# Performance work log

Hardware: AMD Instinct MI355X
Metric: run time of the kernel (lower is better)

Reference implementation:

```python
import jax, jax.numpy as jnp
import numpy as np

NUM_Q = 1000
NUM_PID = 5000
DIM_S = 128
SIZE_M = 50
B, T = 64, 200


def setup_inputs() -> dict:
    key = jax.random.key(0)
    ks = jax.random.split(key, 16)
    s = 1.0 / np.sqrt(DIM_S)
    inp = {
        "q": jax.random.randint(ks[0], (B, T), 0, NUM_Q),
        "r": jax.random.randint(ks[1], (B, T), 0, 2),
        "pid": jax.random.randint(ks[2], (B, T), 0, NUM_PID),
        "pid_emb": jax.random.normal(ks[3], (NUM_PID, DIM_S), jnp.float32),
        "k_emb": jax.random.normal(ks[4], (NUM_Q, DIM_S), jnp.float32),
        "v_emb": jax.random.normal(ks[5], (NUM_Q * 2, DIM_S), jnp.float32),
        "Mk": jax.random.normal(ks[6], (SIZE_M, DIM_S), jnp.float32) * np.sqrt(2.0 / DIM_S),
        "Mv0": jax.random.normal(ks[7], (SIZE_M, DIM_S), jnp.float32) * np.sqrt(2.0 / DIM_S),
        "f_W": jax.random.normal(ks[8], (DIM_S, 2 * DIM_S), jnp.float32) * s,
        "f_b": jnp.zeros((DIM_S,), jnp.float32),
        "p_W": jax.random.normal(ks[9], (1, DIM_S), jnp.float32) * s,
        "p_b": jnp.zeros((1,), jnp.float32),
        "e_W": jax.random.normal(ks[10], (DIM_S, DIM_S), jnp.float32) * s,
        "e_b": jnp.zeros((DIM_S,), jnp.float32),
        "a_W": jax.random.normal(ks[11], (DIM_S, DIM_S), jnp.float32) * s,
        "a_b": jnp.zeros((DIM_S,), jnp.float32),
    }
    return inp


def reference(q, r, pid, pid_emb, k_emb, v_emb, Mk, Mv0, f_W, f_b, p_W, p_b, e_W, e_b, a_W, a_b):
    x = q + NUM_Q * r                         # [B,T] combined q/answer index
    p_e = pid_emb[pid]                        # [B,T,D]
    k = k_emb[q] + p_e                        # [B,T,D]
    v = v_emb[x] + p_e                        # [B,T,D]
    w = jax.nn.softmax(jnp.einsum("btd,md->btm", k, Mk), axis=-1)  # [B,T,M]
    e = jax.nn.sigmoid(jnp.einsum("btd,od->bto", v, e_W) + e_b)    # [B,T,D]
    a = jnp.tanh(jnp.einsum("btd,od->bto", v, a_W) + a_b)          # [B,T,D]

    def step(Mvt, wea):
        wt, et, at = wea                      # [B,M], [B,D], [B,D]
        we = wt[:, :, None]
        Mvt = Mvt * (1.0 - we * et[:, None, :]) + we * at[:, None, :]
        return Mvt, Mvt

    Mv0_b = jnp.broadcast_to(Mv0, (q.shape[0], SIZE_M, DIM_S))
    _, Mv_seq = jax.lax.scan(
        step, Mv0_b,
        (jnp.swapaxes(w, 0, 1), jnp.swapaxes(e, 0, 1), jnp.swapaxes(a, 0, 1)))
    Mv = jnp.concatenate([Mv0_b[:, None], jnp.swapaxes(Mv_seq, 0, 1)], axis=1)  # [B,T+1,M,D]

    read = jnp.einsum("btm,btmd->btd", w, Mv[:, :-1])   # read before each write
    f = jnp.tanh(jnp.einsum("btd,od->bto", jnp.concatenate([read, k], axis=-1), f_W) + f_b)
    p = jax.nn.sigmoid(jnp.einsum("btd,od->bto", f, p_W) + p_b)[..., 0]  # [B,T]
    return (p, Mv)
```

## Files before the change

### kernel.cpp

```cpp
#include <hip/hip_runtime.h>
#include <math.h>

#define BB 64
#define TT 200
#define NUMQ 1000
#define DIMS 128
#define SIZEM 50
#define NROWS (BB*TT)
#define NCH 8
#define CL  25

__global__ __launch_bounds__(256) void k_kernel(
    const int* __restrict__ qv, const int* __restrict__ pidv,
    const float* __restrict__ k_emb, const float* __restrict__ pid_emb,
    float* __restrict__ kout)
{
    int i = blockIdx.x * 256 + threadIdx.x;
    int row = i >> 5;
    int d4  = i & 31;
    int qq = qv[row];
    int pp = pidv[row];
    float4 kvv = ((const float4*)(k_emb  + (size_t)qq * DIMS))[d4];
    float4 pvv = ((const float4*)(pid_emb + (size_t)pp * DIMS))[d4];
    float4 o;
    o.x = kvv.x + pvv.x; o.y = kvv.y + pvv.y;
    o.z = kvv.z + pvv.z; o.w = kvv.w + pvv.w;
    ((float4*)kout)[i] = o;
}

__global__ __launch_bounds__(256) void w_kernel(
    const float* __restrict__ k, const float* __restrict__ Mk,
    float* __restrict__ wout)
{
    __shared__ float MkT[DIMS * SIZEM];
    int tid = threadIdx.x;
    for (int idx = tid; idx < SIZEM * DIMS; idx += 256) {
        int m = idx >> 7;
        int d = idx & 127;
        MkT[d * SIZEM + m] = Mk[idx];
    }
    __syncthreads();

    int wave = tid >> 6;
    int lane = tid & 63;
    int m = (lane < SIZEM) ? lane : (SIZEM - 1);
    int gw = blockIdx.x * 4 + wave;

    for (int row = gw; row < NROWS; row += 256 * 4) {
        const float* kr = k + (size_t)row * DIMS;
        float acc = 0.f;
        #pragma unroll 4
        for (int d = 0; d < DIMS; d++) {
            acc = fmaf(kr[d], MkT[d * SIZEM + m], acc);
        }
        float val = (lane < SIZEM) ? acc : -INFINITY;
        #pragma unroll
        for (int off = 32; off >= 1; off >>= 1)
            val = fmaxf(val, __shfl_xor(val, off));
        float ex = (lane < SIZEM) ? __expf(acc - val) : 0.f;
        float s = ex;
        #pragma unroll
        for (int off = 32; off >= 1; off >>= 1)
            s += __shfl_xor(s, off);
        if (lane < SIZEM)
            wout[(size_t)row * SIZEM + lane] = ex / s;
    }
}

__global__ __launch_bounds__(256) void ea_kernel(
    const int* __restrict__ qv, const int* __restrict__ rv, const int* __restrict__ pidv,
    const float* __restrict__ v_emb, const float* __restrict__ pid_emb,
    const float* __restrict__ e_W, const float* __restrict__ e_b,
    const float* __restrict__ a_W, const float* __restrict__ a_b,
    float* __restrict__ e_out, float* __restrict__ a_out)
{
    __shared__ float vb[32][DIMS];
    int tid = threadIdx.x;
    int o   = tid & 127;
    int sel = tid >> 7;
    int r0  = blockIdx.x * 32;

    for (int idx = tid; idx < 32 * DIMS; idx += 256) {
        int r = idx >> 7, d = idx & 127;
        int row = r0 + r;
        int x = qv[row] + NUMQ * rv[row];
        vb[r][d] = v_emb[(size_t)x * DIMS + d] + pid_emb[(size_t)pidv[row] * DIMS + d];
    }
    __syncthreads();

    float acc[32];
    #pragma unroll
    for (int r = 0; r < 32; r++) acc[r] = 0.f;

    const float* W = sel ? a_W : e_W;
    const float* wrow = W + (size_t)o * DIMS;
    for (int d = 0; d < DIMS; d += 4) {
        float4 wv = *(const float4*)(wrow + d);
        #pragma unroll
        for (int r = 0; r < 32; r++) {
            float4 v4 = *(const float4*)(&vb[r][d]);
            acc[r] = fmaf(v4.x, wv.x, acc[r]);
            acc[r] = fmaf(v4.y, wv.y, acc[r]);
            acc[r] = fmaf(v4.z, wv.z, acc[r]);
            acc[r] = fmaf(v4.w, wv.w, acc[r]);
        }
    }
    float bo = sel ? a_b[o] : e_b[o];
    float* outp = sel ? a_out : e_out;
    #pragma unroll
    for (int r = 0; r < 32; r++) {
        float x = acc[r] + bo;
        float y = sel ? tanhf(x) : 1.f / (1.f + __expf(-x));
        outp[(size_t)(r0 + r) * DIMS + o] = y;
    }
}

__global__ __launch_bounds__(128) void compose_kernel(
    const float* __restrict__ w, const float* __restrict__ e, const float* __restrict__ a,
    float* __restrict__ Abuf, float* __restrict__ Bbuf)
{
    int b = blockIdx.x >> 3;
    int c = blockIdx.x & 7;
    int d = threadIdx.x;

    float A[SIZEM], Bv[SIZEM];
    #pragma unroll
    for (int m = 0; m < SIZEM; m++) { A[m] = 1.f; Bv[m] = 0.f; }

    const float* wr = w + ((size_t)b * TT + c * CL) * SIZEM;
    const float* er = e + ((size_t)b * TT + c * CL) * DIMS + d;
    const float* ar = a + ((size_t)b * TT + c * CL) * DIMS + d;

    for (int t = 0; t < CL; t++) {
        float ed = er[(size_t)t * DIMS];
        float ad = ar[(size_t)t * DIMS];
        const float* wt = wr + (size_t)t * SIZEM;
        #pragma unroll
        for (int m = 0; m < SIZEM; m++) {
            float wv = wt[m];
            float t1 = wv * ed;
            A[m]  = fmaf(-A[m], t1, A[m]);
            Bv[m] = fmaf(-Bv[m], t1, fmaf(wv, ad, Bv[m]));
        }
    }
    float* Ao = Abuf + ((size_t)b * NCH + c) * SIZEM * DIMS + d;
    float* Bo = Bbuf + ((size_t)b * NCH + c) * SIZEM * DIMS + d;
    #pragma unroll
    for (int m = 0; m < SIZEM; m++) {
        Ao[(size_t)m * DIMS] = A[m];
        Bo[(size_t)m * DIMS] = Bv[m];
    }
}

__global__ __launch_bounds__(256) void boundary_kernel(
    const float* __restrict__ Abuf, const float* __restrict__ Bbuf,
    const float* __restrict__ Mv0, float* __restrict__ sstart)
{
    int b = blockIdx.x / 25;
    int g = blockIdx.x % 25;
    int flat = g * 256 + threadIdx.x;
    float s = Mv0[flat];
    #pragma unroll
    for (int c = 0; c < NCH; c++) {
        size_t off = ((size_t)b * NCH + c) * (SIZEM * DIMS) + flat;
        sstart[off] = s;
        float A  = Abuf[off];
        float Bv = Bbuf[off];
        s = fmaf(A, s, Bv);
    }
}

__global__ __launch_bounds__(128) void expand_kernel(
    const float* __restrict__ w, const float* __restrict__ e, const float* __restrict__ a,
    const float* __restrict__ sstart,
    float* __restrict__ mv_out,
    float* __restrict__ read_out)
{
    int b = blockIdx.x >> 3;
    int c = blockIdx.x & 7;
    int d = threadIdx.x;

    float s[SIZEM];
    const float* ss = sstart + ((size_t)b * NCH + c) * (SIZEM * DIMS) + d;
    #pragma unroll
    for (int m = 0; m < SIZEM; m++) s[m] = ss[(size_t)m * DIMS];

    float* mvb = mv_out + (size_t)b * (TT + 1) * SIZEM * DIMS;
    if (c == 0) {
        #pragma unroll
        for (int m = 0; m < SIZEM; m++)
            mvb[(size_t)m * DIMS + d] = s[m];
    }

    const float* wr = w + ((size_t)b * TT + c * CL) * SIZEM;
    const float* er = e + ((size_t)b * TT + c * CL) * DIMS + d;
    const float* ar = a + ((size_t)b * TT + c * CL) * DIMS + d;
    float*       rr = read_out + ((size_t)b * TT + c * CL) * DIMS + d;

    float ed = er[0];
    float ad = ar[0];
    for (int t = 0; t < CL; t++) {
        int tn = (t + 1 < CL) ? t + 1 : t;
        float edn = er[(size_t)tn * DIMS];
        float adn = ar[(size_t)tn * DIMS];

        const float* wt = wr + (size_t)t * SIZEM;
        float* mvt = mvb + (size_t)(c * CL + t + 1) * SIZEM * DIMS + d;
        float pr = 0.f;
        #pragma unroll
        for (int m = 0; m < SIZEM; m++) {
            float wv = wt[m];
            pr = fmaf(wv, s[m], pr);
            float t1 = wv * ed;
            s[m] = fmaf(-s[m], t1, fmaf(wv, ad, s[m]));
            mvt[(size_t)m * DIMS] = s[m];
        }
        rr[(size_t)t * DIMS] = pr;
        ed = edn; ad = adn;
    }
}

__global__ __launch_bounds__(256) void fp_kernel(
    const float* __restrict__ readb, const float* __restrict__ k,
    const float* __restrict__ f_W, const float* __restrict__ f_b,
    const float* __restrict__ p_W, const float* __restrict__ p_b,
    float* __restrict__ p_out)
{
    __shared__ float rk[32][256];
    __shared__ float pred[4][16];
    int tid = threadIdx.x;
    int o  = tid & 127;
    int rh = tid >> 7;
    int r0 = blockIdx.x * 32;

    for (int idx = tid; idx < 32 * 256; idx += 256) {
        int r = idx >> 8, dd = idx & 255;
        size_t row = (size_t)(r0 + r);
        rk[r][dd] = (dd < 128) ? readb[row * 128 + dd] : k[row * 128 + (dd - 128)];
    }
    __syncthreads();

    float acc[16];
    #pragma unroll
    for (int i = 0; i < 16; i++) acc[i] = 0.f;

    const float* wrow = f_W + (size_t)o * 256;
    for (int dd = 0; dd < 256; dd += 4) {
        float4 wv = *(const float4*)(wrow + dd);
        #pragma unroll
        for (int i = 0; i < 16; i++) {
            int r = rh * 16 + i;
            float4 v4 = *(const float4*)(&rk[r][dd]);
            acc[i] = fmaf(v4.x, wv.x, acc[i]);
            acc[i] = fmaf(v4.y, wv.y, acc[i]);
            acc[i] = fmaf(v4.z, wv.z, acc[i]);
            acc[i] = fmaf(v4.w, wv.w, acc[i]);
        }
    }

    int wave = tid >> 6;
    float fb = f_b[o];
    float pw = p_W[o];
    float pb = p_b[0];
    #pragma unroll
    for (int i = 0; i < 16; i++) {
        float fv = tanhf(acc[i] + fb);
        float v = fv * pw;
        #pragma unroll
        for (int off = 32; off >= 1; off >>= 1)
            v += __shfl_xor(v, off);
        if ((tid & 63) == 0) pred[wave][i] = v;
    }
    __syncthreads();
    if (tid < 32) {
        int h = tid >> 4, ri = tid & 15;
        float sum = pred[2 * h][ri] + pred[2 * h + 1][ri];
        p_out[r0 + tid] = 1.f / (1.f + __expf(-(sum + pb)));
    }
}

extern "C" void kernel_launch(void* const* d_in, const int* in_sizes, int n_in,
                              void* d_out, int out_size, void* d_ws, size_t ws_size,
                              hipStream_t stream) {
    const int*   qv      = (const int*)d_in[0];
    const int*   rv      = (const int*)d_in[1];
    const int*   pidv    = (const int*)d_in[2];
    const float* pid_emb = (const float*)d_in[3];
    const float* k_emb   = (const float*)d_in[4];
    const float* v_emb   = (const float*)d_in[5];
    const float* Mk      = (const float*)d_in[6];
    const float* Mv0     = (const float*)d_in[7];
    const float* f_W     = (const float*)d_in[8];
    const float* f_b     = (const float*)d_in[9];
    const float* p_W     = (const float*)d_in[10];
    const float* p_b     = (const float*)d_in[11];
    const float* e_W     = (const float*)d_in[12];
    const float* e_b     = (const float*)d_in[13];
    const float* a_W     = (const float*)d_in[14];
    const float* a_b     = (const float*)d_in[15];

    float* out    = (float*)d_out;
    float* p_out  = out;
    float* mv_out = out + NROWS;

    float* ws = (float*)d_ws;
    float* k_buf    = ws;
    float* w_buf    = ws +  1638400;
    float* e_buf    = ws +  2278400;
    float* a_buf    = ws +  3916800;
    float* read_buf = ws +  5555200;
    float* A_buf    = ws +  7193600;
    float* B_buf    = ws + 10470400;
    float* s_start  = ws + 13747200;

    k_kernel<<<NROWS * 32 / 256, 256, 0, stream>>>(qv, pidv, k_emb, pid_emb, k_buf);
    w_kernel<<<256, 256, 0, stream>>>(k_buf, Mk, w_buf);
    ea_kernel<<<NROWS / 32, 256, 0, stream>>>(qv, rv, pidv, v_emb, pid_emb,
                                              e_W, e_b, a_W, a_b, e_buf, a_buf);
    compose_kernel<<<BB * NCH, 128, 0, stream>>>(w_buf, e_buf, a_buf, A_buf, B_buf);
    boundary_kernel<<<BB * 25, 256, 0, stream>>>(A_buf, B_buf, Mv0, s_start);
    expand_kernel<<<BB * NCH, 128, 0, stream>>>(w_buf, e_buf, a_buf, s_start,
                                                mv_out, read_buf);
    fp_kernel<<<NROWS / 32, 256, 0, stream>>>(read_buf, k_buf, f_W, f_b, p_W, p_b, p_out);
}
```

Before: 532.0 us.

## Fold chunk-boundary scan into expand kernel and tile w_kernel rows per wave

The separate boundary kernel is removed. Each expand block now rebuilds its starting memory state by applying the preceding chunks' affine (A,B) transforms to Mv0 itself, which saves a launch and the s_start write/read round trip. The cost is redundant work: later chunks re-read up to seven chunks of A/B. Separately, w_kernel now has each wave compute four rows at once, sharing each MkT shared-memory load across four accumulators, and launches 800 blocks so every row is covered exactly once.

```diff
diff --git a/kernel.cpp b/kernel.cpp
--- a/kernel.cpp
+++ b/kernel.cpp
@@ -44,27 +44,39 @@
     int wave = tid >> 6;
     int lane = tid & 63;
     int m = (lane < SIZEM) ? lane : (SIZEM - 1);
-    int gw = blockIdx.x * 4 + wave;
-
-    for (int row = gw; row < NROWS; row += 256 * 4) {
-        const float* kr = k + (size_t)row * DIMS;
-        float acc = 0.f;
-        #pragma unroll 4
-        for (int d = 0; d < DIMS; d++) {
-            acc = fmaf(kr[d], MkT[d * SIZEM + m], acc);
-        }
-        float val = (lane < SIZEM) ? acc : -INFINITY;
-        #pragma unroll
-        for (int off = 32; off >= 1; off >>= 1)
-            val = fmaxf(val, __shfl_xor(val, off));
-        float ex = (lane < SIZEM) ? __expf(acc - val) : 0.f;
-        float s = ex;
-        #pragma unroll
-        for (int off = 32; off >= 1; off >>= 1)
-            s += __shfl_xor(s, off);
-        if (lane < SIZEM)
-            wout[(size_t)row * SIZEM + lane] = ex / s;
-    }
+    int g = blockIdx.x * 4 + wave;
+
+    int row0 = __builtin_amdgcn_readfirstlane(g * 4);
+    const float* k0 = k + (size_t)row0 * DIMS;
+
+    float a0 = 0.f, a1 = 0.f, a2 = 0.f, a3 = 0.f;
+    #pragma unroll 8
+    for (int d = 0; d < DIMS; d++) {
+        float mk = MkT[d * SIZEM + m];
+        a0 = fmaf(k0[d],            mk, a0);
+        a1 = fmaf(k0[DIMS + d],     mk, a1);
+        a2 = fmaf(k0[2 * DIMS + d], mk, a2);
+        a3 = fmaf(k0[3 * DIMS + d], mk, a3);
+    }
+
+    #define SOFTMAX_STORE(ACC, RI) { \
+        float val = (lane < SIZEM) ? (ACC) : -INFINITY; \
+        _Pragma("unroll") \
+        for (int off = 32; off >= 1; off >>= 1) \
+            val = fmaxf(val, __shfl_xor(val, off)); \
+        float ex = (lane < SIZEM) ? __expf((ACC) - val) : 0.f; \
+        float ss = ex; \
+        _Pragma("unroll") \
+        for (int off = 32; off >= 1; off >>= 1) \
+            ss += __shfl_xor(ss, off); \
+        if (lane < SIZEM) \
+            wout[(size_t)(row0 + (RI)) * SIZEM + lane] = ex / ss; }
+
+    SOFTMAX_STORE(a0, 0)
+    SOFTMAX_STORE(a1, 1)
+    SOFTMAX_STORE(a2, 2)
+    SOFTMAX_STORE(a3, 3)
+    #undef SOFTMAX_STORE
 }
 
 __global__ __launch_bounds__(256) void ea_kernel(
@@ -152,27 +164,10 @@
     }
 }
 
-__global__ __launch_bounds__(256) void boundary_kernel(
-    const float* __restrict__ Abuf, const float* __restrict__ Bbuf,
-    const float* __restrict__ Mv0, float* __restrict__ sstart)
-{
-    int b = blockIdx.x / 25;
-    int g = blockIdx.x % 25;
-    int flat = g * 256 + threadIdx.x;
-    float s = Mv0[flat];
-    #pragma unroll
-    for (int c = 0; c < NCH; c++) {
-        size_t off = ((size_t)b * NCH + c) * (SIZEM * DIMS) + flat;
-        sstart[off] = s;
-        float A  = Abuf[off];
-        float Bv = Bbuf[off];
-        s = fmaf(A, s, Bv);
-    }
-}
-
 __global__ __launch_bounds__(128) void expand_kernel(
     const float* __restrict__ w, const float* __restrict__ e, const float* __restrict__ a,
-    const float* __restrict__ sstart,
+    const float* __restrict__ Abuf, const float* __restrict__ Bbuf,
+    const float* __restrict__ Mv0,
     float* __restrict__ mv_out,
     float* __restrict__ read_out)
 {
@@ -181,9 +176,16 @@
     int d = threadIdx.x;
 
     float s[SIZEM];
-    const float* ss = sstart + ((size_t)b * NCH + c) * (SIZEM * DIMS) + d;
-    #pragma unroll
-    for (int m = 0; m < SIZEM; m++) s[m] = ss[(size_t)m * DIMS];
+    #pragma unroll
+    for (int m = 0; m < SIZEM; m++) s[m] = Mv0[(size_t)m * DIMS + d];
+
+    for (int cc = 0; cc < c; cc++) {
+        const float* Ao = Abuf + ((size_t)b * NCH + cc) * (SIZEM * DIMS) + d;
+        const float* Bo = Bbuf + ((size_t)b * NCH + cc) * (SIZEM * DIMS) + d;
+        #pragma unroll
+        for (int m = 0; m < SIZEM; m++)
+            s[m] = fmaf(Ao[(size_t)m * DIMS], s[m], Bo[(size_t)m * DIMS]);
+    }
 
     float* mvb = mv_out + (size_t)b * (TT + 1) * SIZEM * DIMS;
     if (c == 0) {
@@ -311,15 +313,13 @@
     float* read_buf = ws +  5555200;
     float* A_buf    = ws +  7193600;
     float* B_buf    = ws + 10470400;
-    float* s_start  = ws + 13747200;
 
     k_kernel<<<NROWS * 32 / 256, 256, 0, stream>>>(qv, pidv, k_emb, pid_emb, k_buf);
-    w_kernel<<<256, 256, 0, stream>>>(k_buf, Mk, w_buf);
+    w_kernel<<<800, 256, 0, stream>>>(k_buf, Mk, w_buf);
     ea_kernel<<<NROWS / 32, 256, 0, stream>>>(qv, rv, pidv, v_emb, pid_emb,
                                               e_W, e_b, a_W, a_b, e_buf, a_buf);
     compose_kernel<<<BB * NCH, 128, 0, stream>>>(w_buf, e_buf, a_buf, A_buf, B_buf);
-    boundary_kernel<<<BB * 25, 256, 0, stream>>>(A_buf, B_buf, Mv0, s_start);
-    expand_kernel<<<BB * NCH, 128, 0, stream>>>(w_buf, e_buf, a_buf, s_start,
-                                                mv_out, read_buf);
+    expand_kernel<<<BB * NCH, 128, 0, stream>>>(w_buf, e_buf, a_buf, A_buf, B_buf,
+                                                Mv0, mv_out, read_buf);
     fp_kernel<<<NROWS / 32, 256, 0, stream>>>(read_buf, k_buf, f_W, f_b, p_W, p_b, p_out);
 }
```

New measurement: 505.8 us. 1.05x faster.
